# Optimization experiments

Measured on AMD Instinct MI355X. Metric: run time of the kernel, lower is better.

## Reference

```python
import jax, jax.numpy as jnp
import numpy as np

V, E, H, O = 32000, 512, 1024, 8   # vocab, embed_dim, hidden_dim, output_dim
B, T = 64, 512
PAD = 1  # padding_idx=1 in nn.Embedding


def setup_inputs() -> dict:
    key = jax.random.key(0)
    ks = jax.random.split(key, 8)
    s = 1.0 / np.sqrt(H)  # torch LSTM init scale
    x = jax.random.randint(ks[0], (B, T), 0, V)
    W_emb = jax.random.normal(ks[1], (V, E), dtype=jnp.float32)
    W_emb = W_emb.at[PAD].set(0.0)  # padding row is zero
    W_ih = jax.random.uniform(ks[2], (4 * H, E), jnp.float32, -s, s)
    W_hh = jax.random.uniform(ks[3], (4 * H, H), jnp.float32, -s, s)
    b_ih = jax.random.uniform(ks[4], (4 * H,), jnp.float32, -s, s)
    b_hh = jax.random.uniform(ks[5], (4 * H,), jnp.float32, -s, s)
    W_out = jax.random.uniform(ks[6], (O, H), jnp.float32, -s, s)
    b_out = jax.random.uniform(ks[7], (O,), jnp.float32, -s, s)
    return {"x": x, "W_emb": W_emb, "W_ih": W_ih, "W_hh": W_hh,
            "b_ih": b_ih, "b_hh": b_hh, "W_out": W_out, "b_out": b_out}


def _lstm_scan(emb_tbe, W_ih, W_hh, b_ih, b_hh):
    # emb_tbe: [T, B, E] -> hidden states [T, B, H]; torch gate order i,f,g,o
    Hh = W_hh.shape[1]
    b = b_ih + b_hh

    def step(carry, x_t):
        h, c = carry
        z = x_t @ W_ih.T + h @ W_hh.T + b  # [B, 4H]
        i, f, g, o = jnp.split(z, 4, axis=-1)
        c = jax.nn.sigmoid(f) * c + jax.nn.sigmoid(i) * jnp.tanh(g)
        h = jax.nn.sigmoid(o) * jnp.tanh(c)
        return (h, c), h

    h0 = jnp.zeros((emb_tbe.shape[1], Hh), emb_tbe.dtype)
    _, hs = jax.lax.scan(step, (h0, h0), emb_tbe)
    return hs


def reference(x, W_emb, W_ih, W_hh, b_ih, b_hh, W_out, b_out):
    Bsz = x.shape[0]
    emb = W_emb[x]                                   # [B, T, E]
    hs = _lstm_scan(emb.transpose(1, 0, 2), W_ih, W_hh, b_ih, b_hh)
    outputs = hs.transpose(1, 0, 2)                  # [B, T, H]
    pad = (x == PAD)
    outputs = jnp.where(pad[..., None], 0.0, outputs)  # masked_fill_
    lengths = jnp.sum(~pad, axis=1)                  # non-pad token counts
    final = outputs[jnp.arange(Bsz), lengths - 1]    # [B, H]
    # Dropout(p=0.5) is identity in eval mode
    logits = final @ W_out.T + b_out                 # [B, O]
    return logits
```

## Files before the change

kernel.cpp:

```cpp
#include <hip/hip_runtime.h>

typedef short bf16x8 __attribute__((ext_vector_type(8)));
typedef float f32x4  __attribute__((ext_vector_type(4)));
typedef unsigned long long u64;

#define MFMA16(a, b, c) __builtin_amdgcn_mfma_f32_16x16x32_bf16((a), (b), (c), 0, 0, 0)
#define AT_LD(p, o)    __hip_atomic_load((p), (o), __HIP_MEMORY_SCOPE_AGENT)
#define AT_ST(p, v, o) __hip_atomic_store((p), (v), (o), __HIP_MEMORY_SCOPE_AGENT)
#define AT_ADD(p, v, o) __hip_atomic_fetch_add((p), (v), (o), __HIP_MEMORY_SCOPE_AGENT)
#define WG_LD(p) __hip_atomic_load((p), __ATOMIC_RELAXED, __HIP_MEMORY_SCOPE_WORKGROUP)
#define WG_ST(p, v) __hip_atomic_store((p), (v), __ATOMIC_RELAXED, __HIP_MEMORY_SCOPE_WORKGROUP)

#define HSLOT 67584

__device__ __forceinline__ unsigned short f2bf(float f) {
  union { float f; unsigned u; } v; v.f = f;
  unsigned u = v.u;
  u += 0x7fffu + ((u >> 16) & 1u);
  return (unsigned short)(u >> 16);
}
__device__ __forceinline__ float bf2f(unsigned short h) {
  union { unsigned u; float f; } v; v.u = ((unsigned)h) << 16;
  return v.f;
}
__device__ __forceinline__ float sigf(float x) { return 1.f / (1.f + __expf(-x)); }
__device__ __forceinline__ float tanh_(float x) {
  x = fminf(15.f, fmaxf(-15.f, x));
  float e = __expf(2.f * x);
  return (e - 1.f) / (e + 1.f);
}

__device__ __forceinline__ void gbar_gemm(unsigned* bar, unsigned target) {
  __syncthreads();
  if (threadIdx.x == 0) {
    unsigned arr = AT_ADD(bar + 8256, 1u, __ATOMIC_RELEASE);
    if (arr == target * 128u - 1u) AT_ST(bar + 8320, target, __ATOMIC_RELEASE);
    while (AT_LD(bar + 8320, __ATOMIC_RELAXED) < target) __builtin_amdgcn_s_sleep(4);
    asm volatile("" ::: "memory");
  }
  __syncthreads();
}

__global__ void k_conv(const float* __restrict__ wih, const float* __restrict__ whh,
                       const float* __restrict__ wemb,
                       unsigned short* __restrict__ oih, unsigned short* __restrict__ ohh,
                       unsigned short* __restrict__ oemb) {
  const size_t NIH = (size_t)4096 * 512, NHH = (size_t)4096 * 1024;
  const size_t NE = (size_t)32000 * 512;
  size_t i0 = ((size_t)blockIdx.x * blockDim.x + threadIdx.x) * 4;
  size_t gs = (size_t)gridDim.x * blockDim.x * 4;
  for (size_t j = i0; j < NIH; j += gs) {
    float4 v = *(const float4*)(wih + j);
    uint2 pk;
    pk.x = (unsigned)f2bf(v.x) | ((unsigned)f2bf(v.y) << 16);
    pk.y = (unsigned)f2bf(v.z) | ((unsigned)f2bf(v.w) << 16);
    *(uint2*)(oih + j) = pk;
  }
  for (size_t j = i0; j < NHH; j += gs) {
    float4 v = *(const float4*)(whh + j);
    uint2 pk;
    pk.x = (unsigned)f2bf(v.x) | ((unsigned)f2bf(v.y) << 16);
    pk.y = (unsigned)f2bf(v.z) | ((unsigned)f2bf(v.w) << 16);
    *(uint2*)(ohh + j) = pk;
  }
  if (oemb)
    for (size_t j = i0; j < NE; j += gs) {
      float4 v = *(const float4*)(wemb + j);
      uint2 pk;
      pk.x = (unsigned)f2bf(v.x) | ((unsigned)f2bf(v.y) << 16);
      pk.y = (unsigned)f2bf(v.z) | ((unsigned)f2bf(v.w) << 16);
      *(uint2*)(oemb + j) = pk;
    }
}

__global__ void k_tsel(const int* __restrict__ x, int* __restrict__ tsel,
                       int* __restrict__ padsel) {
  int b = threadIdx.x >> 3, j = threadIdx.x & 7;
  int c = 0;
  for (int t = j * 64; t < j * 64 + 64; ++t) c += (x[b * 512 + t] != 1) ? 1 : 0;
  c += __shfl_xor(c, 1);
  c += __shfl_xor(c, 2);
  c += __shfl_xor(c, 4);
  if (j == 0) {
    int ts = (c - 1) & 511;
    tsel[b] = ts;
    padsel[b] = (x[b * 512 + ts] == 1) ? 1 : 0;
  }
}

__global__ void k_logits(const float* __restrict__ finalb, const float* __restrict__ Wout,
                         const float* __restrict__ bout, float* __restrict__ out) {
  int tid = threadIdx.x;
  for (int e = tid; e < 512; e += 256) {
    int b = e >> 3, o = e & 7;
    const float* f = finalb + (size_t)b * 1024;
    const float* w = Wout + (size_t)o * 1024;
    float s = 0.f;
    for (int k = 0; k < 1024; ++k) s += f[k] * w[k];
    out[e] = s + bout[o];
  }
}

struct SmemT {
  unsigned tok;
  union {
    struct { unsigned short sW[32][1032]; } rec;
    struct { unsigned short A[128][72]; unsigned short Bt[256][72]; } g;
    struct { unsigned short zs[128][136]; } zst;
  } u;
  unsigned short pad_force_one_wg_per_cu[8192];
};

__global__ __launch_bounds__(256, 1) void k_main(
    const int* __restrict__ x, const float* __restrict__ Wemb,
    const float* __restrict__ bih, const float* __restrict__ bhh,
    const unsigned short* __restrict__ Wihb, const unsigned short* __restrict__ Whhb,
    const unsigned short* __restrict__ wembb,
    unsigned short* __restrict__ hr, float* __restrict__ finalb,
    const int* __restrict__ tsel, const int* __restrict__ padsel,
    unsigned short* __restrict__ zxr, unsigned* __restrict__ bar, int chunkT,
    int nslot) {
  __shared__ SmemT smem;
  const int wg = blockIdx.x, tid = threadIdx.x;
  const int wave = tid >> 6, lane = tid & 63;
  const int l15 = lane & 15, lg = lane >> 4;
  unsigned* gemm_done = bar + 8384;
  unsigned* rec_done  = bar + 8448;
  const f32x4 fz = {0.f, 0.f, 0.f, 0.f};
  const int nChunks = 512 / chunkT;
  const size_t slotE = (size_t)chunkT * 64 * 4096;
  if (tid == 65535) smem.pad_force_one_wg_per_cu[0] = 0;

  if (wg < 128) {
    if (tid == 0) smem.tok = 0;
    for (int e = tid; e < 32 * 128; e += 256) {
      int n = e >> 7, kq = (e & 127) << 3;
      int coll = (n < 16) ? 2 * (n >> 2) : 2 * ((n - 16) >> 2) + 1;
      int grow = (n & 3) * 1024 + wg * 8 + coll;
      *(uint4*)&smem.u.rec.sW[n][kq] = *(const uint4*)(Whhb + (size_t)grow * 1024 + kq);
    }
    const int my_b = wave * 16 + l15;
    const int c0 = wg * 8 + 2 * lg;
    float biasv[2][4];
#pragma unroll
    for (int i = 0; i < 2; ++i)
#pragma unroll
      for (int g = 0; g < 4; ++g)
        biasv[i][g] = bih[g * 1024 + c0 + i] + bhh[g * 1024 + c0 + i];
    const int my_tsel = tsel[my_b];
    const int my_pad = padsel[my_b];
    const size_t hwe = (size_t)wave * 16384 + (size_t)wg * 128 + (size_t)l15 * 8 + 2 * lg;
    const size_t hre = (size_t)wave * 16384 + (size_t)lg * 128 + (size_t)l15 * 8;
    float cc0 = 0.f, cc1 = 0.f;

    AT_ST((unsigned*)hr + (wg * 256 + tid), 0u, __ATOMIC_RELAXED);
    __syncthreads();
    if (tid == 0) AT_ST(bar + wg * 64, 1u, __ATOMIC_RELAXED);

    for (int ch = 0; ch < nChunks; ++ch) {
      const int t0 = ch * chunkT;
      const unsigned short* zxbase = zxr + (size_t)(ch % nslot) * slotE;
      if (tid == 0) {
        while (AT_LD(gemm_done, __ATOMIC_RELAXED) < (unsigned)(ch + 1))
          __builtin_amdgcn_s_sleep(2);
        (void)AT_LD(gemm_done, __ATOMIC_ACQUIRE);
        asm volatile("" ::: "memory");
      }
      __syncthreads();
      union { uint4 u4; unsigned short s[8]; } vv;
      vv.u4 = *(const uint4*)(zxbase + (size_t)my_b * 4096 + c0 * 4);

      for (int tl = 0; tl < chunkT; ++tl) {
        const int t = t0 + tl;
        const unsigned need = (unsigned)t + 1u;

        if (wave == 0) {
          const unsigned* f0 = bar + (lane * 2) * 64;
          const unsigned* f1 = bar + (lane * 2 + 1) * 64;
          for (;;) {
            int ok = (AT_LD(f0, __ATOMIC_RELAXED) >= need) &&
                     (AT_LD(f1, __ATOMIC_RELAXED) >= need);
            if (__all(ok)) break;
            __builtin_amdgcn_s_sleep(1);
          }
          if (lane == 0) WG_ST(&smem.tok, need);
        } else {
          while (WG_LD(&smem.tok) < need) __builtin_amdgcn_s_sleep(1);
        }
        asm volatile("" ::: "memory");

        const unsigned short* hp = hr + (size_t)(t & 15) * HSLOT + hre;
        f32x4 r0 = fz, r1 = fz;
        bf16x8 hf[32];
#pragma unroll
        for (int ks = 0; ks < 32; ++ks) hf[ks] = *(const bf16x8*)(hp + (size_t)ks * 512);
#pragma unroll
        for (int ks = 0; ks < 32; ++ks) {
          int ko = ks * 32 + (lg << 3);
          bf16x8 a0 = *(const bf16x8*)&smem.u.rec.sW[l15][ko];
          bf16x8 a1 = *(const bf16x8*)&smem.u.rec.sW[16 + l15][ko];
          r0 = MFMA16(a0, hf[ks], r0);
          r1 = MFMA16(a1, hf[ks], r1);
        }

        float z00 = r0[0] + biasv[0][0] + bf2f(vv.s[0]);
        float z01 = r0[1] + biasv[0][1] + bf2f(vv.s[1]);
        float z02 = r0[2] + biasv[0][2] + bf2f(vv.s[2]);
        float z03 = r0[3] + biasv[0][3] + bf2f(vv.s[3]);
        float z10 = r1[0] + biasv[1][0] + bf2f(vv.s[4]);
        float z11 = r1[1] + biasv[1][1] + bf2f(vv.s[5]);
        float z12 = r1[2] + biasv[1][2] + bf2f(vv.s[6]);
        float z13 = r1[3] + biasv[1][3] + bf2f(vv.s[7]);

        cc0 = sigf(z01) * cc0 + sigf(z00) * tanh_(z02);
        cc1 = sigf(z11) * cc1 + sigf(z10) * tanh_(z12);
        float h0 = sigf(z03) * tanh_(cc0);
        float h1 = sigf(z13) * tanh_(cc1);

        if (t == my_tsel) {
          finalb[(size_t)my_b * 1024 + c0]     = my_pad ? 0.f : h0;
          finalb[(size_t)my_b * 1024 + c0 + 1] = my_pad ? 0.f : h1;
        }
        unsigned hp32 = (unsigned)f2bf(h0) | ((unsigned)f2bf(h1) << 16);
        AT_ST((unsigned*)(hr + (size_t)((t + 1) & 15) * HSLOT + hwe), hp32,
              __ATOMIC_RELAXED);

        if (tl + 1 < chunkT) {
          vv.u4 = *(const uint4*)(zxbase + (size_t)((tl + 1) * 64 + my_b) * 4096 + c0 * 4);
        }
        __syncthreads();
        if (tid == 0) AT_ST(bar + wg * 64, need + 1u, __ATOMIC_RELAXED);
      }
      if (wg == 0 && tid == 0) AT_ST(rec_done, (unsigned)(ch + 1), __ATOMIC_RELAXED);
    }
  } else {
    const int gw = wg - 128;
    unsigned gt = 0;
    for (int ch = 0; ch < nChunks; ++ch) {
      if (tid == 0 && ch >= nslot) {
        while (AT_LD(rec_done, __ATOMIC_RELAXED) < (unsigned)(ch - nslot + 1))
          __builtin_amdgcn_s_sleep(8);
        asm volatile("" ::: "memory");
      }
      __syncthreads();
      const int t0 = ch * chunkT;
      unsigned short* zx = zxr + (size_t)(ch % nslot) * slotE;
      const int pmN = chunkT >> 1;
      const int npatch = pmN * 16;
      for (int p = gw; p < npatch; p += 128) {
        const int pm = p % pmN;
        const int n0 = (p / pmN) * 256;
        f32x4 acc[8][4];
#pragma unroll
        for (int mt = 0; mt < 8; ++mt)
#pragma unroll
          for (int nt = 0; nt < 4; ++nt) acc[mt][nt] = fz;
        for (int kc = 0; kc < 512; kc += 64) {
          __syncthreads();
          {
            int r = tid >> 1, half = (tid & 1) << 5;
            int tl = pm * 2 + (r >> 6), b = r & 63;
            int erow = x[b * 512 + t0 + tl];
            if (wembb) {
              const unsigned short* srcp = wembb + (size_t)erow * 512 + kc + half;
#pragma unroll
              for (int j = 0; j < 32; j += 8)
                *(uint4*)&smem.u.g.A[r][half + j] = *(const uint4*)(srcp + j);
            } else {
              const float* srcp = Wemb + (size_t)erow * 512 + kc + half;
#pragma unroll
              for (int j = 0; j < 32; j += 4) {
                float4 v = *(const float4*)(srcp + j);
                uint2 pk;
                pk.x = (unsigned)f2bf(v.x) | ((unsigned)f2bf(v.y) << 16);
                pk.y = (unsigned)f2bf(v.z) | ((unsigned)f2bf(v.w) << 16);
                *(uint2*)&smem.u.g.A[r][half + j] = pk;
              }
            }
          }
          {
            int zcx = n0 + tid;
            int wrow = (zcx & 3) * 1024 + (zcx >> 2);
            const unsigned short* srcp = Wihb + (size_t)wrow * 512 + kc;
#pragma unroll
            for (int j = 0; j < 64; j += 8)
              *(uint4*)&smem.u.g.Bt[tid][j] = *(const uint4*)(srcp + j);
          }
          __syncthreads();
#pragma unroll
          for (int ks = 0; ks < 64; ks += 32) {
            bf16x8 af[8];
#pragma unroll
            for (int mt = 0; mt < 8; ++mt)
              af[mt] = *(const bf16x8*)&smem.u.g.A[mt * 16 + l15][ks + (lg << 3)];
#pragma unroll
            for (int nt = 0; nt < 4; ++nt) {
              bf16x8 bfr =
                  *(const bf16x8*)&smem.u.g.Bt[(wave * 4 + nt) * 16 + l15][ks + (lg << 3)];
#pragma unroll
              for (int mt = 0; mt < 8; ++mt)
                acc[mt][nt] = MFMA16(af[mt], bfr, acc[mt][nt]);
            }
          }
        }
#pragma unroll
        for (int h = 0; h < 2; ++h) {
          __syncthreads();
          if ((wave >> 1) == h) {
#pragma unroll
            for (int mt = 0; mt < 8; ++mt)
#pragma unroll
              for (int nt = 0; nt < 4; ++nt)
#pragma unroll
                for (int r = 0; r < 4; ++r)
                  smem.u.zst.zs[mt * 16 + (lg << 2) + r][(wave & 1) * 64 + nt * 16 + l15] =
                      f2bf(acc[mt][nt][r]);
          }
          __syncthreads();
          int m = tid >> 1, qq = (tid & 1) << 6;
          int tl2 = pm * 2 + (m >> 6), bb = m & 63;
          unsigned short* dst = zx + ((size_t)(tl2 * 64 + bb)) * 4096 + n0 + h * 128 + qq;
#pragma unroll
          for (int j = 0; j < 64; j += 8)
            *(uint4*)(dst + j) = *(const uint4*)&smem.u.zst.zs[m][qq + j];
        }
      }
      gbar_gemm(bar, ++gt);
      if (wg == 128 && tid == 0) AT_ST(gemm_done, gt, __ATOMIC_RELAXED);
    }
  }
}

extern "C" void kernel_launch(void* const* d_in, const int* in_sizes, int n_in,
                              void* d_out, int out_size, void* d_ws, size_t ws_size,
                              hipStream_t stream) {
  (void)in_sizes; (void)n_in; (void)out_size;
  const int*   x    = (const int*)  d_in[0];
  const float* Wemb = (const float*)d_in[1];
  const float* Wih  = (const float*)d_in[2];
  const float* Whh  = (const float*)d_in[3];
  const float* bih  = (const float*)d_in[4];
  const float* bhh  = (const float*)d_in[5];
  const float* Wout = (const float*)d_in[6];
  const float* bout = (const float*)d_in[7];
  float* out = (float*)d_out;
  char* ws = (char*)d_ws;

  constexpr size_t OFF_WIH = 0;
  constexpr size_t OFF_WHH = OFF_WIH + (size_t)4096 * 512 * 2;
  constexpr size_t OFF_HR  = OFF_WHH + (size_t)4096 * 1024 * 2;
  constexpr size_t OFF_FIN = OFF_HR + (size_t)16 * HSLOT * 2;
  constexpr size_t OFF_TS  = OFF_FIN + (size_t)64 * 1024 * 4;
  constexpr size_t OFF_PS  = OFF_TS + 4096;
  constexpr size_t OFF_BAR = OFF_PS + 4096;
  constexpr size_t OFF_WEB = OFF_BAR + 40960;
  constexpr size_t WEB_SZ  = (size_t)32000 * 512 * 2;
  constexpr size_t SLOT_SZ = (size_t)16 * 64 * 4096 * 2;

  int chunkT = 16;
  bool wbf = true;
  int nslot = 2;
  if (OFF_WEB + WEB_SZ + 2 * SLOT_SZ <= ws_size) {
    nslot = (int)((ws_size - OFF_WEB - WEB_SZ) / SLOT_SZ);
    if (nslot > 32) nslot = 32;
  } else if (OFF_WEB + 2 * SLOT_SZ <= ws_size) {
    wbf = false;
    nslot = (int)((ws_size - OFF_WEB) / SLOT_SZ);
    if (nslot > 32) nslot = 32;
  } else {
    wbf = false;
    while (chunkT > 2 &&
           OFF_WEB + (size_t)2 * chunkT * 64 * 4096 * 2 > ws_size)
      chunkT >>= 1;
  }
  const size_t OFF_ZX = OFF_WEB + (wbf ? WEB_SZ : 0);

  unsigned short* wihb  = (unsigned short*)(ws + OFF_WIH);
  unsigned short* whhb  = (unsigned short*)(ws + OFF_WHH);
  unsigned short* hr    = (unsigned short*)(ws + OFF_HR);
  float* finalb         = (float*)(ws + OFF_FIN);
  int* tsel             = (int*)(ws + OFF_TS);
  int* padsel           = (int*)(ws + OFF_PS);
  unsigned* bar         = (unsigned*)(ws + OFF_BAR);
  unsigned short* wembb = wbf ? (unsigned short*)(ws + OFF_WEB) : (unsigned short*)nullptr;
  unsigned short* zxr   = (unsigned short*)(ws + OFF_ZX);

  hipMemsetAsync(ws + OFF_BAR, 0, 40960, stream);
  k_conv<<<2048, 256, 0, stream>>>(Wih, Whh, Wemb, wihb, whhb, wembb);
  k_tsel<<<1, 512, 0, stream>>>(x, tsel, padsel);
  k_main<<<256, 256, 0, stream>>>(x, Wemb, bih, bhh, wihb, whhb, wembb, hr, finalb,
                                  tsel, padsel, zxr, bar, chunkT, nslot);
  k_logits<<<1, 256, 0, stream>>>(finalb, Wout, bout, out);
}
```

Measured before the change: 3.156 ms.

## Split recurrent workgroups into two independent batch chains with per-chain flags

Doubles the workgroup size to 512 threads and splits the 64-row batch into two independent chains of four waves. Each chain has its own cross-workgroup flag array, LDS token and completion counter, so the two halves of the batch no longer wait on each other's step barrier. Each wave now computes one gate tile (one MFMA chain instead of two), which shortens per-step latency. A wave-level LDS counter replaces __syncthreads before the flag is published. The GEMM workgroups keep their 256-thread logic by masking thread ids, and now wait on both chains' done counters. The cost is more polling traffic and the extra 256 threads idling in the GEMM workgroups.

After: 2.911 ms. 7.8% less time.

```diff
diff --git a/kernel.cpp b/kernel.cpp
--- a/kernel.cpp
+++ b/kernel.cpp
@@ -8,8 +8,8 @@
 #define AT_LD(p, o)    __hip_atomic_load((p), (o), __HIP_MEMORY_SCOPE_AGENT)
 #define AT_ST(p, v, o) __hip_atomic_store((p), (v), (o), __HIP_MEMORY_SCOPE_AGENT)
 #define AT_ADD(p, v, o) __hip_atomic_fetch_add((p), (v), (o), __HIP_MEMORY_SCOPE_AGENT)
-#define WG_LD(p) __hip_atomic_load((p), __ATOMIC_RELAXED, __HIP_MEMORY_SCOPE_WORKGROUP)
-#define WG_ST(p, v) __hip_atomic_store((p), (v), __ATOMIC_RELAXED, __HIP_MEMORY_SCOPE_WORKGROUP)
+#define WG_LD(p) __hip_atomic_load((p), __ATOMIC_ACQUIRE, __HIP_MEMORY_SCOPE_WORKGROUP)
+#define WG_ST(p, v) __hip_atomic_store((p), (v), __ATOMIC_RELEASE, __HIP_MEMORY_SCOPE_WORKGROUP)
 
 #define HSLOT 67584
 
@@ -33,9 +33,9 @@
 __device__ __forceinline__ void gbar_gemm(unsigned* bar, unsigned target) {
   __syncthreads();
   if (threadIdx.x == 0) {
-    unsigned arr = AT_ADD(bar + 8256, 1u, __ATOMIC_RELEASE);
-    if (arr == target * 128u - 1u) AT_ST(bar + 8320, target, __ATOMIC_RELEASE);
-    while (AT_LD(bar + 8320, __ATOMIC_RELAXED) < target) __builtin_amdgcn_s_sleep(4);
+    unsigned arr = AT_ADD(bar + 16512, 1u, __ATOMIC_RELEASE);
+    if (arr == target * 128u - 1u) AT_ST(bar + 16576, target, __ATOMIC_RELEASE);
+    while (AT_LD(bar + 16576, __ATOMIC_RELAXED) < target) __builtin_amdgcn_s_sleep(4);
     asm volatile("" ::: "memory");
   }
   __syncthreads();
@@ -102,7 +102,8 @@
 }
 
 struct SmemT {
-  unsigned tok;
+  unsigned tok[2];
+  unsigned cnt[2];
   union {
     struct { unsigned short sW[32][1032]; } rec;
     struct { unsigned short A[128][72]; unsigned short Bt[256][72]; } g;
@@ -111,7 +112,7 @@
   unsigned short pad_force_one_wg_per_cu[8192];
 };
 
-__global__ __launch_bounds__(256, 1) void k_main(
+__global__ __launch_bounds__(512, 1) void k_main(
     const int* __restrict__ x, const float* __restrict__ Wemb,
     const float* __restrict__ bih, const float* __restrict__ bhh,
     const unsigned short* __restrict__ Wihb, const unsigned short* __restrict__ Whhb,
@@ -124,122 +125,139 @@
   const int wg = blockIdx.x, tid = threadIdx.x;
   const int wave = tid >> 6, lane = tid & 63;
   const int l15 = lane & 15, lg = lane >> 4;
-  unsigned* gemm_done = bar + 8384;
-  unsigned* rec_done  = bar + 8448;
+  unsigned* gemm_done = bar + 16640;
   const f32x4 fz = {0.f, 0.f, 0.f, 0.f};
   const int nChunks = 512 / chunkT;
   const size_t slotE = (size_t)chunkT * 64 * 4096;
   if (tid == 65535) smem.pad_force_one_wg_per_cu[0] = 0;
 
   if (wg < 128) {
-    if (tid == 0) smem.tok = 0;
-    for (int e = tid; e < 32 * 128; e += 256) {
-      int n = e >> 7, kq = (e & 127) << 3;
+    const int chain = wave >> 2;
+    const int wv = wave & 3;
+    const int btile = chain * 2 + (wv >> 1);
+    const int mtile = wv & 1;
+    const int my_b = btile * 16 + l15;
+    const int col_local = 2 * lg + mtile;
+    const int cg = wg * 8 + col_local;
+    unsigned* myflags = bar + chain * 8192;
+    unsigned* recdone = bar + 16704 + chain * 64;
+
+    if (tid == 0) { smem.tok[0] = 0; smem.tok[1] = 0; smem.cnt[0] = 0; smem.cnt[1] = 0; }
+    for (int e = tid; e < 32 * 64; e += 512) {
+      int n = e >> 6, kq = (e & 63) << 4;
       int coll = (n < 16) ? 2 * (n >> 2) : 2 * ((n - 16) >> 2) + 1;
       int grow = (n & 3) * 1024 + wg * 8 + coll;
       *(uint4*)&smem.u.rec.sW[n][kq] = *(const uint4*)(Whhb + (size_t)grow * 1024 + kq);
+      *(uint4*)&smem.u.rec.sW[n][kq + 8] =
+          *(const uint4*)(Whhb + (size_t)grow * 1024 + kq + 8);
     }
-    const int my_b = wave * 16 + l15;
-    const int c0 = wg * 8 + 2 * lg;
-    float biasv[2][4];
-#pragma unroll
-    for (int i = 0; i < 2; ++i)
-#pragma unroll
-      for (int g = 0; g < 4; ++g)
-        biasv[i][g] = bih[g * 1024 + c0 + i] + bhh[g * 1024 + c0 + i];
+    float biasv[4];
+#pragma unroll
+    for (int g = 0; g < 4; ++g) biasv[g] = bih[g * 1024 + cg] + bhh[g * 1024 + cg];
     const int my_tsel = tsel[my_b];
     const int my_pad = padsel[my_b];
-    const size_t hwe = (size_t)wave * 16384 + (size_t)wg * 128 + (size_t)l15 * 8 + 2 * lg;
-    const size_t hre = (size_t)wave * 16384 + (size_t)lg * 128 + (size_t)l15 * 8;
-    float cc0 = 0.f, cc1 = 0.f;
-
-    AT_ST((unsigned*)hr + (wg * 256 + tid), 0u, __ATOMIC_RELAXED);
+    const size_t hwe = (size_t)btile * 16384 + (size_t)wg * 128 + (size_t)l15 * 8 + col_local;
+    const size_t hre = (size_t)btile * 16384 + (size_t)lg * 128 + (size_t)l15 * 8;
+    float cc = 0.f;
+
+    {
+      int e = wg * 512 + tid;
+      if (e < 32768) AT_ST((unsigned*)hr + e, 0u, __ATOMIC_RELAXED);
+    }
     __syncthreads();
-    if (tid == 0) AT_ST(bar + wg * 64, 1u, __ATOMIC_RELAXED);
+    if (wv == 0 && lane == 0) AT_ST(myflags + wg * 64, 1u, __ATOMIC_RELAXED);
 
     for (int ch = 0; ch < nChunks; ++ch) {
       const int t0 = ch * chunkT;
       const unsigned short* zxbase = zxr + (size_t)(ch % nslot) * slotE;
-      if (tid == 0) {
-        while (AT_LD(gemm_done, __ATOMIC_RELAXED) < (unsigned)(ch + 1))
-          __builtin_amdgcn_s_sleep(2);
-        (void)AT_LD(gemm_done, __ATOMIC_ACQUIRE);
-        asm volatile("" ::: "memory");
-      }
-      __syncthreads();
-      union { uint4 u4; unsigned short s[8]; } vv;
-      vv.u4 = *(const uint4*)(zxbase + (size_t)my_b * 4096 + c0 * 4);
+      union { uint2 u2; unsigned short s[4]; } vv;
+      bool vvload = true;
 
       for (int tl = 0; tl < chunkT; ++tl) {
         const int t = t0 + tl;
         const unsigned need = (unsigned)t + 1u;
 
-        if (wave == 0) {
-          const unsigned* f0 = bar + (lane * 2) * 64;
-          const unsigned* f1 = bar + (lane * 2 + 1) * 64;
+        if (wv == 0) {
+          if (tl == 0) {
+            if (lane == 0) {
+              while (AT_LD(gemm_done, __ATOMIC_RELAXED) < (unsigned)(ch + 1))
+                __builtin_amdgcn_s_sleep(2);
+              (void)AT_LD(gemm_done, __ATOMIC_ACQUIRE);
+              asm volatile("" ::: "memory");
+            }
+          }
+          const unsigned* f0 = myflags + (lane * 2) * 64;
+          const unsigned* f1 = myflags + (lane * 2 + 1) * 64;
           for (;;) {
             int ok = (AT_LD(f0, __ATOMIC_RELAXED) >= need) &&
                      (AT_LD(f1, __ATOMIC_RELAXED) >= need);
             if (__all(ok)) break;
             __builtin_amdgcn_s_sleep(1);
           }
-          if (lane == 0) WG_ST(&smem.tok, need);
+          if (lane == 0) WG_ST(&smem.tok[chain], need);
         } else {
-          while (WG_LD(&smem.tok) < need) __builtin_amdgcn_s_sleep(1);
+          while (WG_LD(&smem.tok[chain]) < need) __builtin_amdgcn_s_sleep(1);
         }
         asm volatile("" ::: "memory");
 
+        if (vvload) {
+          vv.u2 = *(const uint2*)(zxbase + (size_t)(tl * 64 + my_b) * 4096 + cg * 4);
+          vvload = false;
+        }
+
         const unsigned short* hp = hr + (size_t)(t & 15) * HSLOT + hre;
-        f32x4 r0 = fz, r1 = fz;
+        f32x4 r0 = fz;
         bf16x8 hf[32];
 #pragma unroll
         for (int ks = 0; ks < 32; ++ks) hf[ks] = *(const bf16x8*)(hp + (size_t)ks * 512);
 #pragma unroll
         for (int ks = 0; ks < 32; ++ks) {
-          int ko = ks * 32 + (lg << 3);
-          bf16x8 a0 = *(const bf16x8*)&smem.u.rec.sW[l15][ko];
-          bf16x8 a1 = *(const bf16x8*)&smem.u.rec.sW[16 + l15][ko];
+          bf16x8 a0 = *(const bf16x8*)&smem.u.rec.sW[mtile * 16 + l15][ks * 32 + (lg << 3)];
           r0 = MFMA16(a0, hf[ks], r0);
-          r1 = MFMA16(a1, hf[ks], r1);
-        }
-
-        float z00 = r0[0] + biasv[0][0] + bf2f(vv.s[0]);
-        float z01 = r0[1] + biasv[0][1] + bf2f(vv.s[1]);
-        float z02 = r0[2] + biasv[0][2] + bf2f(vv.s[2]);
-        float z03 = r0[3] + biasv[0][3] + bf2f(vv.s[3]);
-        float z10 = r1[0] + biasv[1][0] + bf2f(vv.s[4]);
-        float z11 = r1[1] + biasv[1][1] + bf2f(vv.s[5]);
-        float z12 = r1[2] + biasv[1][2] + bf2f(vv.s[6]);
-        float z13 = r1[3] + biasv[1][3] + bf2f(vv.s[7]);
-
-        cc0 = sigf(z01) * cc0 + sigf(z00) * tanh_(z02);
-        cc1 = sigf(z11) * cc1 + sigf(z10) * tanh_(z12);
-        float h0 = sigf(z03) * tanh_(cc0);
-        float h1 = sigf(z13) * tanh_(cc1);
-
-        if (t == my_tsel) {
-          finalb[(size_t)my_b * 1024 + c0]     = my_pad ? 0.f : h0;
-          finalb[(size_t)my_b * 1024 + c0 + 1] = my_pad ? 0.f : h1;
-        }
-        unsigned hp32 = (unsigned)f2bf(h0) | ((unsigned)f2bf(h1) << 16);
-        AT_ST((unsigned*)(hr + (size_t)((t + 1) & 15) * HSLOT + hwe), hp32,
-              __ATOMIC_RELAXED);
+        }
+
+        float z0 = r0[0] + biasv[0] + bf2f(vv.s[0]);
+        float z1 = r0[1] + biasv[1] + bf2f(vv.s[1]);
+        float z2 = r0[2] + biasv[2] + bf2f(vv.s[2]);
+        float z3 = r0[3] + biasv[3] + bf2f(vv.s[3]);
+        cc = sigf(z1) * cc + sigf(z0) * tanh_(z2);
+        float h = sigf(z3) * tanh_(cc);
+
+        if (t == my_tsel) finalb[(size_t)my_b * 1024 + cg] = my_pad ? 0.f : h;
+        __hip_atomic_store(hr + (size_t)((t + 1) & 15) * HSLOT + hwe, f2bf(h),
+                           __ATOMIC_RELAXED, __HIP_MEMORY_SCOPE_AGENT);
 
         if (tl + 1 < chunkT) {
-          vv.u4 = *(const uint4*)(zxbase + (size_t)((tl + 1) * 64 + my_b) * 4096 + c0 * 4);
-        }
-        __syncthreads();
-        if (tid == 0) AT_ST(bar + wg * 64, need + 1u, __ATOMIC_RELAXED);
+          vv.u2 = *(const uint2*)(zxbase + (size_t)((tl + 1) * 64 + my_b) * 4096 + cg * 4);
+        }
+        asm volatile("s_waitcnt vmcnt(0)" ::: "memory");
+        if (lane == 0)
+          __hip_atomic_fetch_add(&smem.cnt[chain], 1u, __ATOMIC_ACQ_REL,
+                                 __HIP_MEMORY_SCOPE_WORKGROUP);
+        if (wv == 0 && lane == 0) {
+          while (__hip_atomic_load(&smem.cnt[chain], __ATOMIC_ACQUIRE,
+                                   __HIP_MEMORY_SCOPE_WORKGROUP) < 4u * need)
+            __builtin_amdgcn_s_sleep(1);
+          AT_ST(myflags + wg * 64, need + 1u, __ATOMIC_RELAXED);
+        }
       }
-      if (wg == 0 && tid == 0) AT_ST(rec_done, (unsigned)(ch + 1), __ATOMIC_RELAXED);
+      if (wv == 0 && lane == 0) AT_ST(recdone, (unsigned)(ch + 1), __ATOMIC_RELAXED);
     }
   } else {
     const int gw = wg - 128;
+    const int t2 = tid & 255;
+    const int wv4 = (tid >> 6) & 3;
+    unsigned* rdA = bar + 16704;
+    unsigned* rdB = bar + 16768;
     unsigned gt = 0;
     for (int ch = 0; ch < nChunks; ++ch) {
       if (tid == 0 && ch >= nslot) {
-        while (AT_LD(rec_done, __ATOMIC_RELAXED) < (unsigned)(ch - nslot + 1))
+        unsigned tgt = (unsigned)(ch - nslot + 1);
+        for (;;) {
+          unsigned a = AT_LD(rdA, __ATOMIC_RELAXED), b = AT_LD(rdB, __ATOMIC_RELAXED);
+          if (a >= tgt && b >= tgt) break;
           __builtin_amdgcn_s_sleep(8);
+        }
         asm volatile("" ::: "memory");
       }
       __syncthreads();
@@ -258,7 +276,7 @@
         for (int kc = 0; kc < 512; kc += 64) {
           __syncthreads();
           {
-            int r = tid >> 1, half = (tid & 1) << 5;
+            int r = t2 >> 1, half = (t2 & 1) << 5;
             int tl = pm * 2 + (r >> 6), b = r & 63;
             int erow = x[b * 512 + t0 + tl];
             if (wembb) {
@@ -279,12 +297,12 @@
             }
           }
           {
-            int zcx = n0 + tid;
+            int zcx = n0 + t2;
             int wrow = (zcx & 3) * 1024 + (zcx >> 2);
             const unsigned short* srcp = Wihb + (size_t)wrow * 512 + kc;
 #pragma unroll
             for (int j = 0; j < 64; j += 8)
-              *(uint4*)&smem.u.g.Bt[tid][j] = *(const uint4*)(srcp + j);
+              *(uint4*)&smem.u.g.Bt[t2][j] = *(const uint4*)(srcp + j);
           }
           __syncthreads();
 #pragma unroll
@@ -296,7 +314,7 @@
 #pragma unroll
             for (int nt = 0; nt < 4; ++nt) {
               bf16x8 bfr =
-                  *(const bf16x8*)&smem.u.g.Bt[(wave * 4 + nt) * 16 + l15][ks + (lg << 3)];
+                  *(const bf16x8*)&smem.u.g.Bt[(wv4 * 4 + nt) * 16 + l15][ks + (lg << 3)];
 #pragma unroll
               for (int mt = 0; mt < 8; ++mt)
                 acc[mt][nt] = MFMA16(af[mt], bfr, acc[mt][nt]);
@@ -306,18 +324,18 @@
 #pragma unroll
         for (int h = 0; h < 2; ++h) {
           __syncthreads();
-          if ((wave >> 1) == h) {
+          if ((wv4 >> 1) == h) {
 #pragma unroll
             for (int mt = 0; mt < 8; ++mt)
 #pragma unroll
               for (int nt = 0; nt < 4; ++nt)
 #pragma unroll
                 for (int r = 0; r < 4; ++r)
-                  smem.u.zst.zs[mt * 16 + (lg << 2) + r][(wave & 1) * 64 + nt * 16 + l15] =
+                  smem.u.zst.zs[mt * 16 + (lg << 2) + r][(wv4 & 1) * 64 + nt * 16 + l15] =
                       f2bf(acc[mt][nt][r]);
           }
           __syncthreads();
-          int m = tid >> 1, qq = (tid & 1) << 6;
+          int m = t2 >> 1, qq = (t2 & 1) << 6;
           int tl2 = pm * 2 + (m >> 6), bb = m & 63;
           unsigned short* dst = zx + ((size_t)(tl2 * 64 + bb)) * 4096 + n0 + h * 128 + qq;
 #pragma unroll
@@ -353,7 +371,7 @@
   constexpr size_t OFF_TS  = OFF_FIN + (size_t)64 * 1024 * 4;
   constexpr size_t OFF_PS  = OFF_TS + 4096;
   constexpr size_t OFF_BAR = OFF_PS + 4096;
-  constexpr size_t OFF_WEB = OFF_BAR + 40960;
+  constexpr size_t OFF_WEB = OFF_BAR + 73728;
   constexpr size_t WEB_SZ  = (size_t)32000 * 512 * 2;
   constexpr size_t SLOT_SZ = (size_t)16 * 64 * 4096 * 2;
 
@@ -385,10 +403,10 @@
   unsigned short* wembb = wbf ? (unsigned short*)(ws + OFF_WEB) : (unsigned short*)nullptr;
   unsigned short* zxr   = (unsigned short*)(ws + OFF_ZX);
 
-  hipMemsetAsync(ws + OFF_BAR, 0, 40960, stream);
+  hipMemsetAsync(ws + OFF_BAR, 0, 73728, stream);
   k_conv<<<2048, 256, 0, stream>>>(Wih, Whh, Wemb, wihb, whhb, wembb);
   k_tsel<<<1, 512, 0, stream>>>(x, tsel, padsel);
-  k_main<<<256, 256, 0, stream>>>(x, Wemb, bih, bhh, wihb, whhb, wembb, hr, finalb,
+  k_main<<<256, 512, 0, stream>>>(x, Wemb, bih, bhh, wihb, whhb, wembb, hr, finalb,
                                   tsel, padsel, zxr, bar, chunkT, nslot);
   k_logits<<<1, 256, 0, stream>>>(finalb, Wout, bout, out);
 }
```
